# Performance work log

Hardware: AMD Instinct MI355X
Metric: run time of the kernel (lower is better)

Reference implementation:

```python
import jax, jax.numpy as jnp
import numpy as np

EPS = 1e-12  # matches torch F.normalize default eps


def _l2_normalize(x, axis):
    n = jnp.sqrt(jnp.sum(x * x, axis=axis, keepdims=True))
    return x / jnp.maximum(n, EPS)


def setup_inputs() -> dict:
    key = jax.random.key(0)
    k1, k2, k3, k4 = jax.random.split(key, 4)
    B, Din, T = 8, 1024, 2048
    Dcb, V = 64, 8192
    z = jax.random.normal(k1, (B, Din, T), dtype=jnp.float32)
    W = jax.random.normal(k2, (Dcb, Din), dtype=jnp.float32) * 0.02
    b = jax.random.normal(k3, (Dcb,), dtype=jnp.float32) * 0.02
    codebook = jax.random.normal(k4, (V, Dcb), dtype=jnp.float32)
    return {"z": z, "W": W, "b": b, "codebook": codebook}


def reference(z, W, b, codebook):
    # in_project: 1x1 Conv1d over channels -> per-timestep linear
    # z: [B, Din, T], W: [Dcb, Din] -> z_e: [B, Dcb, T]
    z_e = jnp.einsum('bct,dc->bdt', z, W) + b[None, :, None]
    B, Dcb, T = z_e.shape
    encodings = z_e.transpose(0, 2, 1).reshape(B * T, Dcb)  # [N, Dcb]
    en = _l2_normalize(encodings, axis=1)
    cn = _l2_normalize(codebook, axis=1)
    # squared L2 distance between unit vectors (kept in the original expanded form)
    dist = (jnp.sum(en * en, axis=1, keepdims=True)
            - 2.0 * (en @ cn.T)
            + jnp.sum(cn * cn, axis=1)[None, :])  # [N, V]
    indices = jnp.argmax(-dist, axis=1).reshape(B, T)
    return indices
```

## Files before the change

### kernel.cpp

```cpp
#include <hip/hip_runtime.h>
#include <math.h>

#define BB    8
#define DIN   1024
#define TT    2048
#define DCB   64
#define VV    8192
#define NN    (BB * TT)
#define EPSN  1e-12f

#define DSPLIT 8
#define CPCHUNK (VV / DSPLIT)
#define TSTEPS  (CPCHUNK / 32)

typedef float f32x4  __attribute__((ext_vector_type(4)));
typedef float f32x16 __attribute__((ext_vector_type(16)));
typedef int   i32x16 __attribute__((ext_vector_type(16)));
typedef _Float16 half8 __attribute__((ext_vector_type(8)));

typedef const __attribute__((address_space(1))) void* gas_ptr;
typedef __attribute__((address_space(3))) void* las_ptr;

__global__ void __launch_bounds__(256) k_prep_cb(const float* __restrict__ cb,
                                                 _Float16* __restrict__ ch,
                                                 _Float16* __restrict__ cl,
                                                 float* __restrict__ c2) {
    int v    = blockIdx.x * 4 + (threadIdx.x >> 6);
    int k    = threadIdx.x & 63;
    float x  = cb[v * DCB + k];
    float s  = x * x;
    #pragma unroll
    for (int off = 32; off; off >>= 1) s += __shfl_xor(s, off, 64);
    float den = fmaxf(sqrtf(s), EPSN);
    float c   = x / den;

    _Float16 h = (_Float16)c;
    float r    = c - (float)h;
    ch[v * DCB + k] = h;
    cl[v * DCB + k] = (_Float16)(r * 2048.0f);

    float s2 = c * c;
    #pragma unroll
    for (int off = 32; off; off >>= 1) s2 += __shfl_xor(s2, off, 64);
    if (k == 0) c2[v] = s2;
}

__global__ void __launch_bounds__(256) k_prep_wt(const float* __restrict__ W,
                                                 float* __restrict__ wt) {
    int i = blockIdx.x * 256 + threadIdx.x;
    int d = i >> 10;
    int c = i & 1023;
    wt[c * DCB + d] = W[d * DIN + c];
}

__global__ void __launch_bounds__(256, 2)
k_gemm_part(const float* __restrict__ z, const float* __restrict__ wt,
            float* __restrict__ part, int kch) {
    __shared__ __align__(1024) float wlds[256 * 64];

    int tid  = threadIdx.x;
    int lane = tid & 63;
    int wv   = tid >> 6;
    int d0   = wv * 16;
    int n0   = blockIdx.x * 256;
    int ks   = blockIdx.y;
    int c0   = ks * kch;
    int b    = n0 >> 11;
    int t0   = (n0 & 2047) + lane * 4;

    {
        const f32x4* wsrc = (const f32x4*)(wt + (size_t)c0 * DCB);
        int ncalls = kch / 16;
        for (int k = 0; k < ncalls; ++k) {
            int ub = k * 256 + wv * 64;
            __builtin_amdgcn_global_load_lds((gas_ptr)(wsrc + ub + lane),
                                             (las_ptr)((f32x4*)wlds + ub), 16, 0, 0);
        }
    }
    asm volatile("s_waitcnt vmcnt(0)" ::: "memory");
    __syncthreads();

    const float* zp = z + (size_t)b * (DIN * TT) + (size_t)c0 * TT + t0;

    f32x4 acc[4][4];
    #pragma unroll
    for (int i = 0; i < 4; ++i)
        #pragma unroll
        for (int j = 0; j < 4; ++j) acc[i][j] = (f32x4)0.0f;

    #pragma unroll 8
    for (int c = 0; c < kch; ++c) {
        f32x4 zv = *(const f32x4*)(zp + (size_t)c * TT);
        const f32x4* wr = (const f32x4*)&wlds[c * DCB + d0];
        f32x4 w0 = wr[0], w1 = wr[1], w2 = wr[2], w3 = wr[3];
        #pragma unroll
        for (int tq = 0; tq < 4; ++tq) {
            float zs = zv[tq];
            acc[tq][0] += w0 * zs;
            acc[tq][1] += w1 * zs;
            acc[tq][2] += w2 * zs;
            acc[tq][3] += w3 * zs;
        }
    }

    float* pp = part + ((size_t)ks * NN + n0 + lane * 4) * DCB + d0;
    #pragma unroll
    for (int tq = 0; tq < 4; ++tq) {
        f32x4* dst = (f32x4*)(pp + (size_t)tq * DCB);
        dst[0] = acc[tq][0];
        dst[1] = acc[tq][1];
        dst[2] = acc[tq][2];
        dst[3] = acc[tq][3];
    }
}

__global__ void __launch_bounds__(256) k_combine(const float* __restrict__ part,
                                                 const float* __restrict__ bias,
                                                 _Float16* __restrict__ eh,
                                                 _Float16* __restrict__ el,
                                                 int ksplit) {
    int gid = blockIdx.x * 256 + threadIdx.x;
    int n   = gid >> 3;
    int d0  = (gid & 7) * 8;

    float ze[8];
    #pragma unroll
    for (int j = 0; j < 8; ++j) ze[j] = bias[d0 + j];

    for (int ks = 0; ks < ksplit; ++ks) {
        const float4* pp = (const float4*)(part + ((size_t)ks * NN + n) * DCB + d0);
        float4 p0 = pp[0], p1 = pp[1];
        ze[0] += p0.x; ze[1] += p0.y; ze[2] += p0.z; ze[3] += p0.w;
        ze[4] += p1.x; ze[5] += p1.y; ze[6] += p1.z; ze[7] += p1.w;
    }

    float ss = 0.0f;
    #pragma unroll
    for (int j = 0; j < 8; ++j) ss = fmaf(ze[j], ze[j], ss);
    ss += __shfl_xor(ss, 1, 64);
    ss += __shfl_xor(ss, 2, 64);
    ss += __shfl_xor(ss, 4, 64);
    float den = fmaxf(sqrtf(ss), EPSN);

    half8 vh, vl;
    #pragma unroll
    for (int j = 0; j < 8; ++j) {
        float x = ze[j] / den;
        _Float16 h = (_Float16)x;
        vh[j] = h;
        vl[j] = (_Float16)((x - (float)h) * 2048.0f);
    }
    *(half8*)&eh[(size_t)n * DCB + d0] = vh;
    *(half8*)&el[(size_t)n * DCB + d0] = vl;
}

__global__ void __launch_bounds__(256)
k_distmax(const _Float16* __restrict__ eh, const _Float16* __restrict__ el,
          const _Float16* __restrict__ chg, const _Float16* __restrict__ clg,
          const float* __restrict__ c2,
          float* __restrict__ pscore, int* __restrict__ pidx) {
    __shared__ __align__(1024) char smem[2][2][4096];

    int tid  = threadIdx.x;
    int w    = tid >> 6;
    int lane = tid & 63;
    int rr   = lane & 31;
    int hhf  = lane >> 5;
    int chunk = blockIdx.y;
    int v0   = chunk * CPCHUNK;
    int m0   = blockIdx.x * 128 + w * 32;

    const char* ehp = (const char*)(eh + (size_t)(m0 + rr) * DCB) + hhf * 16;
    const char* elp = (const char*)(el + (size_t)(m0 + rr) * DCB) + hhf * 16;
    half8 ah0 = *(const half8*)(ehp +  0), ah1 = *(const half8*)(ehp + 32);
    half8 ah2 = *(const half8*)(ehp + 64), ah3 = *(const half8*)(ehp + 96);
    half8 al0 = *(const half8*)(elp +  0), al1 = *(const half8*)(elp + 32);
    half8 al2 = *(const half8*)(elp + 64), al3 = *(const half8*)(elp + 96);
    asm volatile("" : "+v"(ah0), "+v"(ah1), "+v"(ah2), "+v"(ah3),
                      "+v"(al0), "+v"(al1), "+v"(al2), "+v"(al3));

    #define STAGE(b, t)                                                          \
    {                                                                            \
        const char* chs = (const char*)chg + ((size_t)(v0 + (t) * 32)) * 128;    \
        const char* cls = (const char*)clg + ((size_t)(v0 + (t) * 32)) * 128;    \
        _Pragma("unroll")                                                        \
        for (int j = 0; j < 2; ++j) {                                            \
            int cc   = w * 2 + j;                                                \
            int prt  = cc & 3;                                                   \
            int lin  = prt * 1024 + (lane << 4);                                 \
            int so   = lin ^ (((lin >> 7) & 7) << 4);                            \
            const char* gs = (cc < 4 ? chs : cls) + so;                          \
            __builtin_amdgcn_global_load_lds((gas_ptr)gs,                        \
                (las_ptr)&smem[b][cc >= 4][prt * 1024], 16, 0, 0);               \
        }                                                                        \
    }

    STAGE(0, 0);

    f32x16 kz;
    f32x16 best;
    i32x16 bidx;
    #pragma unroll
    for (int i = 0; i < 16; ++i) { kz[i] = 0.0f; best[i] = -INFINITY; bidx[i] = 0; }

    asm volatile("s_waitcnt vmcnt(0)" ::: "memory");
    __syncthreads();

    int lin0 = rr * 128 + hhf * 16;

    for (int t = 0; t < TSTEPS; ++t) {
        int cur = t & 1;
        if (t + 1 < TSTEPS) STAGE(cur ^ 1, t + 1);

        int   vcode = v0 + t * 32 + rr;
        float c2v   = c2[vcode];

        #define SWZ(x) ((x) ^ ((((x) >> 7) & 7) << 4))
        half8 bh0 = *(const half8*)&smem[cur][0][SWZ(lin0 +  0)];
        half8 bh1 = *(const half8*)&smem[cur][0][SWZ(lin0 + 32)];
        half8 bh2 = *(const half8*)&smem[cur][0][SWZ(lin0 + 64)];
        half8 bh3 = *(const half8*)&smem[cur][0][SWZ(lin0 + 96)];
        half8 bl0 = *(const half8*)&smem[cur][1][SWZ(lin0 +  0)];
        half8 bl1 = *(const half8*)&smem[cur][1][SWZ(lin0 + 32)];
        half8 bl2 = *(const half8*)&smem[cur][1][SWZ(lin0 + 64)];
        half8 bl3 = *(const half8*)&smem[cur][1][SWZ(lin0 + 96)];
        #undef SWZ

        f32x16 Ahh, Amid;
        Ahh  = __builtin_amdgcn_mfma_f32_32x32x16_f16(ah0, bh0, kz, 0, 0, 0);
        Amid = __builtin_amdgcn_mfma_f32_32x32x16_f16(ah0, bl0, kz, 0, 0, 0);
        Amid = __builtin_amdgcn_mfma_f32_32x32x16_f16(al0, bh0, Amid, 0, 0, 0);
        Ahh  = __builtin_amdgcn_mfma_f32_32x32x16_f16(ah1, bh1, Ahh, 0, 0, 0);
        Amid = __builtin_amdgcn_mfma_f32_32x32x16_f16(ah1, bl1, Amid, 0, 0, 0);
        Amid = __builtin_amdgcn_mfma_f32_32x32x16_f16(al1, bh1, Amid, 0, 0, 0);
        Ahh  = __builtin_amdgcn_mfma_f32_32x32x16_f16(ah2, bh2, Ahh, 0, 0, 0);
        Amid = __builtin_amdgcn_mfma_f32_32x32x16_f16(ah2, bl2, Amid, 0, 0, 0);
        Amid = __builtin_amdgcn_mfma_f32_32x32x16_f16(al2, bh2, Amid, 0, 0, 0);
        Ahh  = __builtin_amdgcn_mfma_f32_32x32x16_f16(ah3, bh3, Ahh, 0, 0, 0);
        Amid = __builtin_amdgcn_mfma_f32_32x32x16_f16(ah3, bl3, Amid, 0, 0, 0);
        Amid = __builtin_amdgcn_mfma_f32_32x32x16_f16(al3, bh3, Amid, 0, 0, 0);

        #pragma unroll
        for (int i = 0; i < 16; ++i) {
            float dot = fmaf(Amid[i], 4.8828125e-4f, Ahh[i]);
            float s   = fmaf(2.0f, dot, -c2v);
            bool  g   = s > best[i];
            best[i]   = g ? s : best[i];
            bidx[i]   = g ? vcode : bidx[i];
        }

        asm volatile("s_waitcnt vmcnt(0)" ::: "memory");
        __syncthreads();
    }
    #undef STAGE

    #pragma unroll
    for (int i = 0; i < 16; ++i) {
        float bv = best[i];
        int   bi = bidx[i];
        #pragma unroll
        for (int off = 1; off < 32; off <<= 1) {
            float ob = __shfl_xor(bv, off, 64);
            int   oi = __shfl_xor(bi, off, 64);
            if (ob > bv || (ob == bv && oi < bi)) { bv = ob; bi = oi; }
        }
        if (rr == 0) {
            int row = m0 + (i & 3) + 8 * (i >> 2) + 4 * hhf;
            pscore[(size_t)chunk * NN + row] = bv;
            pidx  [(size_t)chunk * NN + row] = bi;
        }
    }
}

__global__ void __launch_bounds__(256) k_reduce(const float* __restrict__ pscore,
                                                const int* __restrict__ pidx,
                                                int* __restrict__ out) {
    int n = blockIdx.x * 256 + threadIdx.x;
    float best = -INFINITY;
    int   bi   = 0;
    #pragma unroll
    for (int c = 0; c < DSPLIT; ++c) {
        float s = pscore[(size_t)c * NN + n];
        int  id = pidx [(size_t)c * NN + n];
        if (s > best) { best = s; bi = id; }
    }
    out[n] = bi;
}

extern "C" void kernel_launch(void* const* d_in, const int* in_sizes, int n_in,
                              void* d_out, int out_size, void* d_ws, size_t ws_size,
                              hipStream_t stream) {
    const float* z  = (const float*)d_in[0];
    const float* W  = (const float*)d_in[1];
    const float* bi = (const float*)d_in[2];
    const float* cb = (const float*)d_in[3];
    int* out = (int*)d_out;

    char* ws = (char*)d_ws;
    _Float16* ch  = (_Float16*)(ws);
    _Float16* cl  = (_Float16*)(ws + 1048576);
    float*    c2  = (float*)   (ws + 2097152);
    float*    wt  = (float*)   (ws + 2129920);
    _Float16* eh  = (_Float16*)(ws + 2392064);
    _Float16* el  = (_Float16*)(ws + 4489216);
    float* pscore = (float*)   (ws + 6586368);
    int*   pidx   = (int*)     (ws + 7110656);
    float* part   = (float*)   (ws + 7634944);

    const size_t need8 = 7634944ULL + (size_t)8 * NN * DCB * 4;
    int ksplit = (ws_size >= need8) ? 8 : 4;
    int kch    = DIN / ksplit;

    hipLaunchKernelGGL(k_prep_cb,   dim3(VV / 4),          dim3(256), 0, stream, cb, ch, cl, c2);
    hipLaunchKernelGGL(k_prep_wt,   dim3(DIN * DCB / 256), dim3(256), 0, stream, W, wt);
    hipLaunchKernelGGL(k_gemm_part, dim3(NN / 256, ksplit), dim3(256), 0, stream, z, wt, part, kch);
    hipLaunchKernelGGL(k_combine,   dim3(NN * 8 / 256),    dim3(256), 0, stream, part, bi, eh, el, ksplit);
    hipLaunchKernelGGL(k_distmax,   dim3(NN / 128, DSPLIT), dim3(256), 0, stream,
                       eh, el, ch, cl, c2, pscore, pidx);
    hipLaunchKernelGGL(k_reduce,    dim3(NN / 256),        dim3(256), 0, stream, pscore, pidx, out);
}
```

Baseline: 129.2 us.

## Triple-buffer codebook tiles, cache c2 in LDS, split mid MFMA chains

Moves the distance-argmax loop from a double-buffered to a triple-buffered LDS pipeline that prefetches two tiles ahead and waits only on the older loads (vmcnt(2)) with raw s_barrier. Each block loads its chunk of the c2 norms into shared memory once, replacing a per-iteration global load. The mixed-precision correction is split into two independent MFMA accumulator chains to shorten the dependent MFMA chain. This costs more LDS and registers, which may lower occupancy, and the hand-written waitcnt and barrier sequence is fragile if wrong.

```diff
diff --git a/kernel.cpp b/kernel.cpp
--- a/kernel.cpp
+++ b/kernel.cpp
@@ -154,12 +154,15 @@
     *(half8*)&el[(size_t)n * DCB + d0] = vl;
 }
 
+#define SWZB(x) ((x) ^ ((((x) >> 7) & 7) << 4))
+
 __global__ void __launch_bounds__(256)
 k_distmax(const _Float16* __restrict__ eh, const _Float16* __restrict__ el,
           const _Float16* __restrict__ chg, const _Float16* __restrict__ clg,
           const float* __restrict__ c2,
           float* __restrict__ pscore, int* __restrict__ pidx) {
-    __shared__ __align__(1024) char smem[2][2][4096];
+    __shared__ __align__(1024) char smem[3][2][4096];
+    __shared__ float c2l[CPCHUNK];
 
     int tid  = threadIdx.x;
     int w    = tid >> 6;
@@ -169,6 +172,11 @@
     int chunk = blockIdx.y;
     int v0   = chunk * CPCHUNK;
     int m0   = blockIdx.x * 128 + w * 32;
+
+    {
+        f32x4 cv = *(const f32x4*)(c2 + v0 + tid * 4);
+        *(f32x4*)&c2l[tid * 4] = cv;
+    }
 
     const char* ehp = (const char*)(eh + (size_t)(m0 + rr) * DCB) + hhf * 16;
     const char* elp = (const char*)(el + (size_t)(m0 + rr) * DCB) + hhf * 16;
@@ -196,6 +204,7 @@
     }
 
     STAGE(0, 0);
+    STAGE(1, 1);
 
     f32x16 kz;
     f32x16 best;
@@ -203,56 +212,67 @@
     #pragma unroll
     for (int i = 0; i < 16; ++i) { kz[i] = 0.0f; best[i] = -INFINITY; bidx[i] = 0; }
 
+    int lin0 = rr * 128 + hhf * 16;
+
+    #define TILE_COMPUTE(BUF, T)                                                 \
+    {                                                                            \
+        int   vcode = v0 + (T) * 32 + rr;                                        \
+        float c2v   = c2l[(T) * 32 + rr];                                        \
+        const char* sh = &smem[BUF][0][0];                                       \
+        const char* sl = &smem[BUF][1][0];                                       \
+        half8 bh0 = *(const half8*)(sh + SWZB(lin0 +  0));                       \
+        half8 bh1 = *(const half8*)(sh + SWZB(lin0 + 32));                       \
+        half8 bh2 = *(const half8*)(sh + SWZB(lin0 + 64));                       \
+        half8 bh3 = *(const half8*)(sh + SWZB(lin0 + 96));                       \
+        half8 bl0 = *(const half8*)(sl + SWZB(lin0 +  0));                       \
+        half8 bl1 = *(const half8*)(sl + SWZB(lin0 + 32));                       \
+        half8 bl2 = *(const half8*)(sl + SWZB(lin0 + 64));                       \
+        half8 bl3 = *(const half8*)(sl + SWZB(lin0 + 96));                       \
+        f32x16 Ahh, Am1, Am2;                                                    \
+        Ahh = __builtin_amdgcn_mfma_f32_32x32x16_f16(ah0, bh0, kz, 0, 0, 0);     \
+        Am1 = __builtin_amdgcn_mfma_f32_32x32x16_f16(ah0, bl0, kz, 0, 0, 0);     \
+        Am2 = __builtin_amdgcn_mfma_f32_32x32x16_f16(al0, bh0, kz, 0, 0, 0);     \
+        Ahh = __builtin_amdgcn_mfma_f32_32x32x16_f16(ah1, bh1, Ahh, 0, 0, 0);    \
+        Am1 = __builtin_amdgcn_mfma_f32_32x32x16_f16(ah1, bl1, Am1, 0, 0, 0);    \
+        Am2 = __builtin_amdgcn_mfma_f32_32x32x16_f16(al1, bh1, Am2, 0, 0, 0);    \
+        Ahh = __builtin_amdgcn_mfma_f32_32x32x16_f16(ah2, bh2, Ahh, 0, 0, 0);    \
+        Am1 = __builtin_amdgcn_mfma_f32_32x32x16_f16(ah2, bl2, Am1, 0, 0, 0);    \
+        Am2 = __builtin_amdgcn_mfma_f32_32x32x16_f16(al2, bh2, Am2, 0, 0, 0);    \
+        Ahh = __builtin_amdgcn_mfma_f32_32x32x16_f16(ah3, bh3, Ahh, 0, 0, 0);    \
+        Am1 = __builtin_amdgcn_mfma_f32_32x32x16_f16(ah3, bl3, Am1, 0, 0, 0);    \
+        Am2 = __builtin_amdgcn_mfma_f32_32x32x16_f16(al3, bh3, Am2, 0, 0, 0);    \
+        _Pragma("unroll")                                                        \
+        for (int i = 0; i < 16; ++i) {                                           \
+            float am  = Am1[i] + Am2[i];                                         \
+            float dot = fmaf(am, 4.8828125e-4f, Ahh[i]);                         \
+            float s   = fmaf(2.0f, dot, -c2v);                                   \
+            bool  g   = s > best[i];                                             \
+            best[i]   = g ? s : best[i];                                         \
+            bidx[i]   = g ? vcode : bidx[i];                                     \
+        }                                                                        \
+    }
+
+    asm volatile("s_waitcnt vmcnt(2) lgkmcnt(0)" ::: "memory");
+    __builtin_amdgcn_s_barrier();
+
+    int cur = 0;
+    #pragma unroll 3
+    for (int t = 0; t < TSTEPS - 2; ++t) {
+        int nb = cur + 2; if (nb >= 3) nb -= 3;
+        STAGE(nb, t + 2);
+        TILE_COMPUTE(cur, t);
+        asm volatile("s_waitcnt vmcnt(2)" ::: "memory");
+        __builtin_amdgcn_s_barrier();
+        cur = (cur == 2) ? 0 : cur + 1;
+    }
+    TILE_COMPUTE(cur, TSTEPS - 2);
     asm volatile("s_waitcnt vmcnt(0)" ::: "memory");
-    __syncthreads();
-
-    int lin0 = rr * 128 + hhf * 16;
-
-    for (int t = 0; t < TSTEPS; ++t) {
-        int cur = t & 1;
-        if (t + 1 < TSTEPS) STAGE(cur ^ 1, t + 1);
-
-        int   vcode = v0 + t * 32 + rr;
-        float c2v   = c2[vcode];
-
-        #define SWZ(x) ((x) ^ ((((x) >> 7) & 7) << 4))
-        half8 bh0 = *(const half8*)&smem[cur][0][SWZ(lin0 +  0)];
-        half8 bh1 = *(const half8*)&smem[cur][0][SWZ(lin0 + 32)];
-        half8 bh2 = *(const half8*)&smem[cur][0][SWZ(lin0 + 64)];
-        half8 bh3 = *(const half8*)&smem[cur][0][SWZ(lin0 + 96)];
-        half8 bl0 = *(const half8*)&smem[cur][1][SWZ(lin0 +  0)];
-        half8 bl1 = *(const half8*)&smem[cur][1][SWZ(lin0 + 32)];
-        half8 bl2 = *(const half8*)&smem[cur][1][SWZ(lin0 + 64)];
-        half8 bl3 = *(const half8*)&smem[cur][1][SWZ(lin0 + 96)];
-        #undef SWZ
-
-        f32x16 Ahh, Amid;
-        Ahh  = __builtin_amdgcn_mfma_f32_32x32x16_f16(ah0, bh0, kz, 0, 0, 0);
-        Amid = __builtin_amdgcn_mfma_f32_32x32x16_f16(ah0, bl0, kz, 0, 0, 0);
-        Amid = __builtin_amdgcn_mfma_f32_32x32x16_f16(al0, bh0, Amid, 0, 0, 0);
-        Ahh  = __builtin_amdgcn_mfma_f32_32x32x16_f16(ah1, bh1, Ahh, 0, 0, 0);
-        Amid = __builtin_amdgcn_mfma_f32_32x32x16_f16(ah1, bl1, Amid, 0, 0, 0);
-        Amid = __builtin_amdgcn_mfma_f32_32x32x16_f16(al1, bh1, Amid, 0, 0, 0);
-        Ahh  = __builtin_amdgcn_mfma_f32_32x32x16_f16(ah2, bh2, Ahh, 0, 0, 0);
-        Amid = __builtin_amdgcn_mfma_f32_32x32x16_f16(ah2, bl2, Amid, 0, 0, 0);
-        Amid = __builtin_amdgcn_mfma_f32_32x32x16_f16(al2, bh2, Amid, 0, 0, 0);
-        Ahh  = __builtin_amdgcn_mfma_f32_32x32x16_f16(ah3, bh3, Ahh, 0, 0, 0);
-        Amid = __builtin_amdgcn_mfma_f32_32x32x16_f16(ah3, bl3, Amid, 0, 0, 0);
-        Amid = __builtin_amdgcn_mfma_f32_32x32x16_f16(al3, bh3, Amid, 0, 0, 0);
-
-        #pragma unroll
-        for (int i = 0; i < 16; ++i) {
-            float dot = fmaf(Amid[i], 4.8828125e-4f, Ahh[i]);
-            float s   = fmaf(2.0f, dot, -c2v);
-            bool  g   = s > best[i];
-            best[i]   = g ? s : best[i];
-            bidx[i]   = g ? vcode : bidx[i];
-        }
-
-        asm volatile("s_waitcnt vmcnt(0)" ::: "memory");
-        __syncthreads();
-    }
+    __builtin_amdgcn_s_barrier();
+    cur = (cur == 2) ? 0 : cur + 1;
+    TILE_COMPUTE(cur, TSTEPS - 1);
+
     #undef STAGE
+    #undef TILE_COMPUTE
 
     #pragma unroll
     for (int i = 0; i < 16; ++i) {
```

New measurement: 140.1 us. 1.08x slower.

## Register-block two row tiles per wave in distmax and stage c2 in LDS

Applied to the files above, without the earlier changes.

Each wave now holds encoder fragments for two 32-row tiles and reuses every codebook fragment read from LDS for both tiles' MFMA chains. The grid's row dimension is halved to match. The c2 norms for the codebook chunk are loaded into shared memory once per block instead of being read from global memory every step. This cuts LDS reads and codebook staging per output row, but raises register use and leaves fewer blocks to spread across CUs. The explicit vmcnt waits before the barriers were also removed, which relies on the barrier to order the async LDS loads.

```diff
diff --git a/kernel.cpp b/kernel.cpp
--- a/kernel.cpp
+++ b/kernel.cpp
@@ -20,6 +20,8 @@
 
 typedef const __attribute__((address_space(1))) void* gas_ptr;
 typedef __attribute__((address_space(3))) void* las_ptr;
+
+#define SWZB(x) ((x) ^ ((((x) >> 7) & 7) << 4))
 
 __global__ void __launch_bounds__(256) k_prep_cb(const float* __restrict__ cb,
                                                  _Float16* __restrict__ ch,
@@ -160,6 +162,7 @@
           const float* __restrict__ c2,
           float* __restrict__ pscore, int* __restrict__ pidx) {
     __shared__ __align__(1024) char smem[2][2][4096];
+    __shared__ float c2l[CPCHUNK];
 
     int tid  = threadIdx.x;
     int w    = tid >> 6;
@@ -168,16 +171,29 @@
     int hhf  = lane >> 5;
     int chunk = blockIdx.y;
     int v0   = chunk * CPCHUNK;
-    int m0   = blockIdx.x * 128 + w * 32;
-
-    const char* ehp = (const char*)(eh + (size_t)(m0 + rr) * DCB) + hhf * 16;
-    const char* elp = (const char*)(el + (size_t)(m0 + rr) * DCB) + hhf * 16;
-    half8 ah0 = *(const half8*)(ehp +  0), ah1 = *(const half8*)(ehp + 32);
-    half8 ah2 = *(const half8*)(ehp + 64), ah3 = *(const half8*)(ehp + 96);
-    half8 al0 = *(const half8*)(elp +  0), al1 = *(const half8*)(elp + 32);
-    half8 al2 = *(const half8*)(elp + 64), al3 = *(const half8*)(elp + 96);
-    asm volatile("" : "+v"(ah0), "+v"(ah1), "+v"(ah2), "+v"(ah3),
-                      "+v"(al0), "+v"(al1), "+v"(al2), "+v"(al3));
+    int mA   = blockIdx.x * 256 + w * 32;
+
+    {
+        f32x4 cv = *(const f32x4*)(c2 + v0 + tid * 4);
+        *(f32x4*)&c2l[tid * 4] = cv;
+    }
+
+    const char* ehpA = (const char*)(eh + (size_t)(mA + rr) * DCB) + hhf * 16;
+    const char* elpA = (const char*)(el + (size_t)(mA + rr) * DCB) + hhf * 16;
+    const char* ehpB = ehpA + 128 * DCB * 2;
+    const char* elpB = elpA + 128 * DCB * 2;
+    half8 aA0 = *(const half8*)(ehpA +  0), aA1 = *(const half8*)(ehpA + 32);
+    half8 aA2 = *(const half8*)(ehpA + 64), aA3 = *(const half8*)(ehpA + 96);
+    half8 lA0 = *(const half8*)(elpA +  0), lA1 = *(const half8*)(elpA + 32);
+    half8 lA2 = *(const half8*)(elpA + 64), lA3 = *(const half8*)(elpA + 96);
+    half8 aB0 = *(const half8*)(ehpB +  0), aB1 = *(const half8*)(ehpB + 32);
+    half8 aB2 = *(const half8*)(ehpB + 64), aB3 = *(const half8*)(ehpB + 96);
+    half8 lB0 = *(const half8*)(elpB +  0), lB1 = *(const half8*)(elpB + 32);
+    half8 lB2 = *(const half8*)(elpB + 64), lB3 = *(const half8*)(elpB + 96);
+    asm volatile("" : "+v"(aA0), "+v"(aA1), "+v"(aA2), "+v"(aA3),
+                      "+v"(lA0), "+v"(lA1), "+v"(lA2), "+v"(lA3),
+                      "+v"(aB0), "+v"(aB1), "+v"(aB2), "+v"(aB3),
+                      "+v"(lB0), "+v"(lB1), "+v"(lB2), "+v"(lB3));
 
     #define STAGE(b, t)                                                          \
     {                                                                            \
@@ -188,7 +204,7 @@
             int cc   = w * 2 + j;                                                \
             int prt  = cc & 3;                                                   \
             int lin  = prt * 1024 + (lane << 4);                                 \
-            int so   = lin ^ (((lin >> 7) & 7) << 4);                            \
+            int so   = SWZB(lin);                                                \
             const char* gs = (cc < 4 ? chs : cls) + so;                          \
             __builtin_amdgcn_global_load_lds((gas_ptr)gs,                        \
                 (las_ptr)&smem[b][cc >= 4][prt * 1024], 16, 0, 0);               \
@@ -198,12 +214,15 @@
     STAGE(0, 0);
 
     f32x16 kz;
-    f32x16 best;
-    i32x16 bidx;
-    #pragma unroll
-    for (int i = 0; i < 16; ++i) { kz[i] = 0.0f; best[i] = -INFINITY; bidx[i] = 0; }
-
-    asm volatile("s_waitcnt vmcnt(0)" ::: "memory");
+    f32x16 bestA, bestB;
+    i32x16 bidxA, bidxB;
+    #pragma unroll
+    for (int i = 0; i < 16; ++i) {
+        kz[i] = 0.0f;
+        bestA[i] = -INFINITY; bidxA[i] = 0;
+        bestB[i] = -INFINITY; bidxB[i] = 0;
+    }
+
     __syncthreads();
 
     int lin0 = rr * 128 + hhf * 16;
@@ -213,51 +232,69 @@
         if (t + 1 < TSTEPS) STAGE(cur ^ 1, t + 1);
 
         int   vcode = v0 + t * 32 + rr;
-        float c2v   = c2[vcode];
-
-        #define SWZ(x) ((x) ^ ((((x) >> 7) & 7) << 4))
-        half8 bh0 = *(const half8*)&smem[cur][0][SWZ(lin0 +  0)];
-        half8 bh1 = *(const half8*)&smem[cur][0][SWZ(lin0 + 32)];
-        half8 bh2 = *(const half8*)&smem[cur][0][SWZ(lin0 + 64)];
-        half8 bh3 = *(const half8*)&smem[cur][0][SWZ(lin0 + 96)];
-        half8 bl0 = *(const half8*)&smem[cur][1][SWZ(lin0 +  0)];
-        half8 bl1 = *(const half8*)&smem[cur][1][SWZ(lin0 + 32)];
-        half8 bl2 = *(const half8*)&smem[cur][1][SWZ(lin0 + 64)];
-        half8 bl3 = *(const half8*)&smem[cur][1][SWZ(lin0 + 96)];
-        #undef SWZ
+        float c2v   = c2l[t * 32 + rr];
+
+        const char* sh = &smem[cur][0][0];
+        const char* sl = &smem[cur][1][0];
+        half8 bh0 = *(const half8*)(sh + SWZB(lin0 +  0));
+        half8 bh1 = *(const half8*)(sh + SWZB(lin0 + 32));
+        half8 bh2 = *(const half8*)(sh + SWZB(lin0 + 64));
+        half8 bh3 = *(const half8*)(sh + SWZB(lin0 + 96));
+        half8 bl0 = *(const half8*)(sl + SWZB(lin0 +  0));
+        half8 bl1 = *(const half8*)(sl + SWZB(lin0 + 32));
+        half8 bl2 = *(const half8*)(sl + SWZB(lin0 + 64));
+        half8 bl3 = *(const half8*)(sl + SWZB(lin0 + 96));
 
         f32x16 Ahh, Amid;
-        Ahh  = __builtin_amdgcn_mfma_f32_32x32x16_f16(ah0, bh0, kz, 0, 0, 0);
-        Amid = __builtin_amdgcn_mfma_f32_32x32x16_f16(ah0, bl0, kz, 0, 0, 0);
-        Amid = __builtin_amdgcn_mfma_f32_32x32x16_f16(al0, bh0, Amid, 0, 0, 0);
-        Ahh  = __builtin_amdgcn_mfma_f32_32x32x16_f16(ah1, bh1, Ahh, 0, 0, 0);
-        Amid = __builtin_amdgcn_mfma_f32_32x32x16_f16(ah1, bl1, Amid, 0, 0, 0);
-        Amid = __builtin_amdgcn_mfma_f32_32x32x16_f16(al1, bh1, Amid, 0, 0, 0);
-        Ahh  = __builtin_amdgcn_mfma_f32_32x32x16_f16(ah2, bh2, Ahh, 0, 0, 0);
-        Amid = __builtin_amdgcn_mfma_f32_32x32x16_f16(ah2, bl2, Amid, 0, 0, 0);
-        Amid = __builtin_amdgcn_mfma_f32_32x32x16_f16(al2, bh2, Amid, 0, 0, 0);
-        Ahh  = __builtin_amdgcn_mfma_f32_32x32x16_f16(ah3, bh3, Ahh, 0, 0, 0);
-        Amid = __builtin_amdgcn_mfma_f32_32x32x16_f16(ah3, bl3, Amid, 0, 0, 0);
-        Amid = __builtin_amdgcn_mfma_f32_32x32x16_f16(al3, bh3, Amid, 0, 0, 0);
+        Ahh  = __builtin_amdgcn_mfma_f32_32x32x16_f16(aA0, bh0, kz, 0, 0, 0);
+        Amid = __builtin_amdgcn_mfma_f32_32x32x16_f16(aA0, bl0, kz, 0, 0, 0);
+        Amid = __builtin_amdgcn_mfma_f32_32x32x16_f16(lA0, bh0, Amid, 0, 0, 0);
+        Ahh  = __builtin_amdgcn_mfma_f32_32x32x16_f16(aA1, bh1, Ahh, 0, 0, 0);
+        Amid = __builtin_amdgcn_mfma_f32_32x32x16_f16(aA1, bl1, Amid, 0, 0, 0);
+        Amid = __builtin_amdgcn_mfma_f32_32x32x16_f16(lA1, bh1, Amid, 0, 0, 0);
+        Ahh  = __builtin_amdgcn_mfma_f32_32x32x16_f16(aA2, bh2, Ahh, 0, 0, 0);
+        Amid = __builtin_amdgcn_mfma_f32_32x32x16_f16(aA2, bl2, Amid, 0, 0, 0);
+        Amid = __builtin_amdgcn_mfma_f32_32x32x16_f16(lA2, bh2, Amid, 0, 0, 0);
+        Ahh  = __builtin_amdgcn_mfma_f32_32x32x16_f16(aA3, bh3, Ahh, 0, 0, 0);
+        Amid = __builtin_amdgcn_mfma_f32_32x32x16_f16(aA3, bl3, Amid, 0, 0, 0);
+        Amid = __builtin_amdgcn_mfma_f32_32x32x16_f16(lA3, bh3, Amid, 0, 0, 0);
+
+        f32x16 Bhh, Bmid;
+        Bhh  = __builtin_amdgcn_mfma_f32_32x32x16_f16(aB0, bh0, kz, 0, 0, 0);
+        Bmid = __builtin_amdgcn_mfma_f32_32x32x16_f16(aB0, bl0, kz, 0, 0, 0);
+        Bmid = __builtin_amdgcn_mfma_f32_32x32x16_f16(lB0, bh0, Bmid, 0, 0, 0);
+        Bhh  = __builtin_amdgcn_mfma_f32_32x32x16_f16(aB1, bh1, Bhh, 0, 0, 0);
+        Bmid = __builtin_amdgcn_mfma_f32_32x32x16_f16(aB1, bl1, Bmid, 0, 0, 0);
+        Bmid = __builtin_amdgcn_mfma_f32_32x32x16_f16(lB1, bh1, Bmid, 0, 0, 0);
+        Bhh  = __builtin_amdgcn_mfma_f32_32x32x16_f16(aB2, bh2, Bhh, 0, 0, 0);
+        Bmid = __builtin_amdgcn_mfma_f32_32x32x16_f16(aB2, bl2, Bmid, 0, 0, 0);
+        Bmid = __builtin_amdgcn_mfma_f32_32x32x16_f16(lB2, bh2, Bmid, 0, 0, 0);
+        Bhh  = __builtin_amdgcn_mfma_f32_32x32x16_f16(aB3, bh3, Bhh, 0, 0, 0);
+        Bmid = __builtin_amdgcn_mfma_f32_32x32x16_f16(aB3, bl3, Bmid, 0, 0, 0);
+        Bmid = __builtin_amdgcn_mfma_f32_32x32x16_f16(lB3, bh3, Bmid, 0, 0, 0);
 
         #pragma unroll
         for (int i = 0; i < 16; ++i) {
-            float dot = fmaf(Amid[i], 4.8828125e-4f, Ahh[i]);
-            float s   = fmaf(2.0f, dot, -c2v);
-            bool  g   = s > best[i];
-            best[i]   = g ? s : best[i];
-            bidx[i]   = g ? vcode : bidx[i];
-        }
-
-        asm volatile("s_waitcnt vmcnt(0)" ::: "memory");
+            float dotA = fmaf(Amid[i], 4.8828125e-4f, Ahh[i]);
+            float sA   = fmaf(2.0f, dotA, -c2v);
+            bool  gA   = sA > bestA[i];
+            bestA[i]   = gA ? sA : bestA[i];
+            bidxA[i]   = gA ? vcode : bidxA[i];
+            float dotB = fmaf(Bmid[i], 4.8828125e-4f, Bhh[i]);
+            float sB   = fmaf(2.0f, dotB, -c2v);
+            bool  gB   = sB > bestB[i];
+            bestB[i]   = gB ? sB : bestB[i];
+            bidxB[i]   = gB ? vcode : bidxB[i];
+        }
+
         __syncthreads();
     }
     #undef STAGE
 
     #pragma unroll
     for (int i = 0; i < 16; ++i) {
-        float bv = best[i];
-        int   bi = bidx[i];
+        float bv = bestA[i];
+        int   bi = bidxA[i];
         #pragma unroll
         for (int off = 1; off < 32; off <<= 1) {
             float ob = __shfl_xor(bv, off, 64);
@@ -265,7 +302,23 @@
             if (ob > bv || (ob == bv && oi < bi)) { bv = ob; bi = oi; }
         }
         if (rr == 0) {
-            int row = m0 + (i & 3) + 8 * (i >> 2) + 4 * hhf;
+            int row = mA + (i & 3) + 8 * (i >> 2) + 4 * hhf;
+            pscore[(size_t)chunk * NN + row] = bv;
+            pidx  [(size_t)chunk * NN + row] = bi;
+        }
+    }
+    #pragma unroll
+    for (int i = 0; i < 16; ++i) {
+        float bv = bestB[i];
+        int   bi = bidxB[i];
+        #pragma unroll
+        for (int off = 1; off < 32; off <<= 1) {
+            float ob = __shfl_xor(bv, off, 64);
+            int   oi = __shfl_xor(bi, off, 64);
+            if (ob > bv || (ob == bv && oi < bi)) { bv = ob; bi = oi; }
+        }
+        if (rr == 0) {
+            int row = mA + 128 + (i & 3) + 8 * (i >> 2) + 4 * hhf;
             pscore[(size_t)chunk * NN + row] = bv;
             pidx  [(size_t)chunk * NN + row] = bi;
         }
@@ -315,7 +368,7 @@
     hipLaunchKernelGGL(k_prep_wt,   dim3(DIN * DCB / 256), dim3(256), 0, stream, W, wt);
     hipLaunchKernelGGL(k_gemm_part, dim3(NN / 256, ksplit), dim3(256), 0, stream, z, wt, part, kch);
     hipLaunchKernelGGL(k_combine,   dim3(NN * 8 / 256),    dim3(256), 0, stream, part, bi, eh, el, ksplit);
-    hipLaunchKernelGGL(k_distmax,   dim3(NN / 128, DSPLIT), dim3(256), 0, stream,
+    hipLaunchKernelGGL(k_distmax,   dim3(NN / 256, DSPLIT), dim3(256), 0, stream,
                        eh, el, ch, cl, c2, pscore, pidx);
     hipLaunchKernelGGL(k_reduce,    dim3(NN / 256),        dim3(256), 0, stream, pscore, pidx, out);
 }
```

Measured after the change: 128.3 us. No clear change (-0.7%).

## Load codebook tiles directly from global memory instead of LDS staging, halve vocab split

Applied to the files above, without the earlier changes.

The distance/argmax kernel drops its double-buffered LDS staging of codebook tiles (global_load_lds plus a barrier every step). Each lane now reads its codebook fragments straight from global memory into registers, with a 2x unrolled loop. The vocabulary split drops from 8 to 4 chunks, so each block loops over twice as many codes and the partial score/index buffers shrink, with workspace offsets updated to match. This removes per-iteration barriers and LDS traffic but relies on L2/cache for codebook reuse across waves and halves grid parallelism.

```diff
diff --git a/kernel.cpp b/kernel.cpp
--- a/kernel.cpp
+++ b/kernel.cpp
@@ -9,7 +9,7 @@
 #define NN    (BB * TT)
 #define EPSN  1e-12f
 
-#define DSPLIT 8
+#define DSPLIT 4
 #define CPCHUNK (VV / DSPLIT)
 #define TSTEPS  (CPCHUNK / 32)
 
@@ -159,8 +159,6 @@
           const _Float16* __restrict__ chg, const _Float16* __restrict__ clg,
           const float* __restrict__ c2,
           float* __restrict__ pscore, int* __restrict__ pidx) {
-    __shared__ __align__(1024) char smem[2][2][4096];
-
     int tid  = threadIdx.x;
     int w    = tid >> 6;
     int lane = tid & 63;
@@ -179,23 +177,8 @@
     asm volatile("" : "+v"(ah0), "+v"(ah1), "+v"(ah2), "+v"(ah3),
                       "+v"(al0), "+v"(al1), "+v"(al2), "+v"(al3));
 
-    #define STAGE(b, t)                                                          \
-    {                                                                            \
-        const char* chs = (const char*)chg + ((size_t)(v0 + (t) * 32)) * 128;    \
-        const char* cls = (const char*)clg + ((size_t)(v0 + (t) * 32)) * 128;    \
-        _Pragma("unroll")                                                        \
-        for (int j = 0; j < 2; ++j) {                                            \
-            int cc   = w * 2 + j;                                                \
-            int prt  = cc & 3;                                                   \
-            int lin  = prt * 1024 + (lane << 4);                                 \
-            int so   = lin ^ (((lin >> 7) & 7) << 4);                            \
-            const char* gs = (cc < 4 ? chs : cls) + so;                          \
-            __builtin_amdgcn_global_load_lds((gas_ptr)gs,                        \
-                (las_ptr)&smem[b][cc >= 4][prt * 1024], 16, 0, 0);               \
-        }                                                                        \
-    }
-
-    STAGE(0, 0);
+    const char* chp = (const char*)chg + ((size_t)(v0 + rr)) * 128 + hhf * 16;
+    const char* clp = (const char*)clg + ((size_t)(v0 + rr)) * 128 + hhf * 16;
 
     f32x16 kz;
     f32x16 best;
@@ -203,28 +186,22 @@
     #pragma unroll
     for (int i = 0; i < 16; ++i) { kz[i] = 0.0f; best[i] = -INFINITY; bidx[i] = 0; }
 
-    asm volatile("s_waitcnt vmcnt(0)" ::: "memory");
-    __syncthreads();
-
-    int lin0 = rr * 128 + hhf * 16;
-
+    #pragma unroll 2
     for (int t = 0; t < TSTEPS; ++t) {
-        int cur = t & 1;
-        if (t + 1 < TSTEPS) STAGE(cur ^ 1, t + 1);
+        const char* bh = chp + (size_t)t * (32 * 128);
+        const char* bl = clp + (size_t)t * (32 * 128);
+
+        half8 bh0 = *(const half8*)(bh +  0);
+        half8 bh1 = *(const half8*)(bh + 32);
+        half8 bh2 = *(const half8*)(bh + 64);
+        half8 bh3 = *(const half8*)(bh + 96);
+        half8 bl0 = *(const half8*)(bl +  0);
+        half8 bl1 = *(const half8*)(bl + 32);
+        half8 bl2 = *(const half8*)(bl + 64);
+        half8 bl3 = *(const half8*)(bl + 96);
 
         int   vcode = v0 + t * 32 + rr;
         float c2v   = c2[vcode];
-
-        #define SWZ(x) ((x) ^ ((((x) >> 7) & 7) << 4))
-        half8 bh0 = *(const half8*)&smem[cur][0][SWZ(lin0 +  0)];
-        half8 bh1 = *(const half8*)&smem[cur][0][SWZ(lin0 + 32)];
-        half8 bh2 = *(const half8*)&smem[cur][0][SWZ(lin0 + 64)];
-        half8 bh3 = *(const half8*)&smem[cur][0][SWZ(lin0 + 96)];
-        half8 bl0 = *(const half8*)&smem[cur][1][SWZ(lin0 +  0)];
-        half8 bl1 = *(const half8*)&smem[cur][1][SWZ(lin0 + 32)];
-        half8 bl2 = *(const half8*)&smem[cur][1][SWZ(lin0 + 64)];
-        half8 bl3 = *(const half8*)&smem[cur][1][SWZ(lin0 + 96)];
-        #undef SWZ
 
         f32x16 Ahh, Amid;
         Ahh  = __builtin_amdgcn_mfma_f32_32x32x16_f16(ah0, bh0, kz, 0, 0, 0);
@@ -248,11 +225,7 @@
             best[i]   = g ? s : best[i];
             bidx[i]   = g ? vcode : bidx[i];
         }
-
-        asm volatile("s_waitcnt vmcnt(0)" ::: "memory");
-        __syncthreads();
-    }
-    #undef STAGE
+    }
 
     #pragma unroll
     for (int i = 0; i < 16; ++i) {
@@ -304,10 +277,10 @@
     _Float16* eh  = (_Float16*)(ws + 2392064);
     _Float16* el  = (_Float16*)(ws + 4489216);
     float* pscore = (float*)   (ws + 6586368);
-    int*   pidx   = (int*)     (ws + 7110656);
-    float* part   = (float*)   (ws + 7634944);
-
-    const size_t need8 = 7634944ULL + (size_t)8 * NN * DCB * 4;
+    int*   pidx   = (int*)     (ws + 6848512);
+    float* part   = (float*)   (ws + 7110656);
+
+    const size_t need8 = 7110656ULL + (size_t)8 * NN * DCB * 4;
     int ksplit = (ws_size >= need8) ? 8 : 4;
     int kch    = DIN / ksplit;
 
```

Result: slower. 179.5 us (+38.9%).
